# Kernel optimization log

Measured on AMD Instinct MI355X. Metric: run time of the kernel, lower is better.

Reference implementation:

```python
import jax, jax.numpy as jnp
import numpy as np

BATCH, SEQ, FEAT, LAYERS = 32, 512, 1024, 2


def setup_inputs() -> dict:
    key = jax.random.key(0)
    ks = jax.random.split(key, 1 + 3 * LAYERS)
    inp = {"x": jax.random.normal(ks[0], (BATCH, SEQ, FEAT), dtype=jnp.float32)}
    scale_i = 1.0 / np.sqrt(FEAT)
    for l in range(LAYERS):
        # flax OptimizedLSTMCell: input dense (no bias) + hidden dense (with bias),
        # both producing 4*features (gates i, f, g, o concatenated).
        inp[f"Wi{l}"] = jax.random.normal(ks[1 + 3 * l], (FEAT, 4 * FEAT), dtype=jnp.float32) * scale_i
        inp[f"Wh{l}"] = jax.random.normal(ks[2 + 3 * l], (FEAT, 4 * FEAT), dtype=jnp.float32) * scale_i
        inp[f"b{l}"] = jnp.zeros((4 * FEAT,), dtype=jnp.float32)
    return inp


def _lstm_layer(x, Wi, Wh, b):
    # x: [B, T, F_in]; returns [B, T, F]
    B = x.shape[0]
    F = Wh.shape[0]
    # Precompute input projections for all steps (one big GEMM): [B, T, 4F]
    xz = jnp.einsum("btf,fg->btg", x, Wi) + b

    def step(carry, xz_t):
        c, h = carry
        z = xz_t + h @ Wh  # [B, 4F]
        i, f, g, o = jnp.split(z, 4, axis=-1)
        c_new = jax.nn.sigmoid(f) * c + jax.nn.sigmoid(i) * jnp.tanh(g)
        h_new = jax.nn.sigmoid(o) * jnp.tanh(c_new)
        return (c_new, h_new), h_new

    init = (jnp.zeros((B, F), x.dtype), jnp.zeros((B, F), x.dtype))
    _, ys = jax.lax.scan(step, init, jnp.swapaxes(xz, 0, 1))  # scan over time
    return jnp.swapaxes(ys, 0, 1)


def reference(x, Wi0, Wh0, b0, Wi1, Wh1, b1):
    y = _lstm_layer(x, Wi0, Wh0, b0)
    y = _lstm_layer(y, Wi1, Wh1, b1)
    return y
```

## Files before the change

### kernel.cpp

```cpp
#include <hip/hip_runtime.h>
#include <hip/hip_bf16.h>
#include <hip/hip_fp16.h>


typedef _Float16 f16x8 __attribute__((ext_vector_type(8)));
typedef __fp16 fp16x2 __attribute__((ext_vector_type(2)));
typedef float f32x4 __attribute__((ext_vector_type(4)));

#define NB 32
#define NTT 512
#define NF 1024
#define NG 4096
#define TFE (NTT * NF)
#define NWG 256
#define NTHR 512

#define W_F16X8 8192
#define W_BYTES (W_F16X8 * 16)
#define ZQSEG 33
#define Z_FLOATS (8 * 16 * ZQSEG)
#define LDS_BYTES (W_BYTES + Z_FLOATS * 4)
#define RINGB 65536
#define MBOX 4096

__device__ __forceinline__ float sigm(float v) { return 1.0f / (1.0f + __expf(-v)); }
__device__ __forceinline__ float tanh_s(float v) {
  float a = fabsf(v);
  float e = __expf(-2.0f * a);
  float t = (1.0f - e) / (1.0f + e);
  return v < 0.0f ? -t : t;
}

__device__ __forceinline__ unsigned pk(float a, float b) {
  union { fp16x2 h2; unsigned u; } c;
  c.h2 = __builtin_amdgcn_cvt_pkrtz(a, b);
  return c.u;
}

__device__ __forceinline__ f16x8 cvt8(f32x4 lo, f32x4 hi) {
  union { unsigned u[4]; f16x8 h8; } u;
  u.u[0] = pk(lo[0], lo[1]);
  u.u[1] = pk(lo[2], lo[3]);
  u.u[2] = pk(hi[0], hi[1]);
  u.u[3] = pk(hi[2], hi[3]);
  return u.h8;
}

__device__ __forceinline__ unsigned ldu(const unsigned* p) {
  unsigned v;
  asm volatile("global_load_dword %0, %1, off sc0 sc1\n\ts_waitcnt vmcnt(0)"
               : "=&v"(v) : "v"(p) : "memory");
  return v;
}

__device__ __forceinline__ void ld4(f16x8 o[4], const char* p) {
  asm volatile("global_load_dwordx4 %0, %4, off sc0 sc1\n\t"
               "global_load_dwordx4 %1, %4, off offset:64 sc0 sc1\n\t"
               "global_load_dwordx4 %2, %4, off offset:128 sc0 sc1\n\t"
               "global_load_dwordx4 %3, %4, off offset:192 sc0 sc1"
               : "=&v"(o[0]), "=&v"(o[1]), "=&v"(o[2]), "=&v"(o[3])
               : "v"(p) : "memory");
}

__global__ __launch_bounds__(NTHR, 1) void lstm_persist(
    const float* __restrict__ x,
    const float* __restrict__ Wi0, const float* __restrict__ Wh0, const float* __restrict__ bv0,
    const float* __restrict__ Wi1, const float* __restrict__ Wh1, const float* __restrict__ bv1,
    float* __restrict__ out, unsigned short* __restrict__ hring_u16,
    unsigned* __restrict__ bar) {
  extern __shared__ char lds[];
  f16x8* Wl = (f16x8*)lds;
  float* Zr = (float*)(lds + W_BYTES);

  const int wg = blockIdx.x;
  const int tid = threadIdx.x;
  const int role = wg >> 7;
  const int fg = wg & 127;
  const int fbase = fg * 8;
  const int w = tid >> 6;
  const int Kq = w >> 1;
  const int mt = w & 1;
  const int lane = tid & 63;
  const int lr = lane & 15;
  const int g = lane >> 4;
  unsigned gen = 0;

  auto arrive = [&]() {
    asm volatile("s_waitcnt vmcnt(0) lgkmcnt(0)" ::: "memory");
    __syncthreads();
    ++gen;
    if (tid == 0)
      asm volatile("global_store_dword %0, %1, off sc0 sc1"
                   :: "v"(&bar[wg * 16]), "v"(gen) : "memory");
    if (wg == 0) {
      if (tid < 64) {
        const unsigned* f0 = &bar[(tid * 4 + 0) * 16];
        const unsigned* f1 = &bar[(tid * 4 + 1) * 16];
        const unsigned* f2 = &bar[(tid * 4 + 2) * 16];
        const unsigned* f3 = &bar[(tid * 4 + 3) * 16];
        for (;;) {
          unsigned v0, v1, v2, v3;
          asm volatile("global_load_dword %0, %4, off sc0 sc1\n\t"
                       "global_load_dword %1, %5, off sc0 sc1\n\t"
                       "global_load_dword %2, %6, off sc0 sc1\n\t"
                       "global_load_dword %3, %7, off sc0 sc1\n\t"
                       "s_waitcnt vmcnt(0)"
                       : "=&v"(v0), "=&v"(v1), "=&v"(v2), "=&v"(v3)
                       : "v"(f0), "v"(f1), "v"(f2), "v"(f3)
                       : "memory");
          if (__all((v0 >= gen) & (v1 >= gen) & (v2 >= gen) & (v3 >= gen))) break;
        }
      }
      __syncthreads();
      if (tid < 256)
        asm volatile("global_store_dword %0, %1, off sc0 sc1"
                     :: "v"(&bar[MBOX + tid * 16]), "v"(gen) : "memory");
      __syncthreads();
    }
  };

  auto waitgen = [&]() {
    const unsigned* mb = &bar[MBOX + wg * 16];
    for (;;) {
      if (ldu(mb) >= gen) break;
      __builtin_amdgcn_s_sleep(1);
    }
  };

  const float* Wi = role ? Wi1 : Wi0;
  const float* Wh = role ? Wh1 : Wh0;
  const float* bv = role ? bv1 : bv0;
  unsigned* h0 = (unsigned*)hring_u16;
  unsigned* h1 = (unsigned*)(hring_u16 + 2 * NB * NF);
  unsigned* hmine = role ? h1 : h0;

  for (int idx = tid; idx < 16384; idx += NTHR) {
    const int k = idx >> 3, chunk = idx & 7;
    const int q = chunk >> 1, half = chunk & 1;
    const float* src = (k < NF) ? (Wi + (size_t)k * NG) : (Wh + (size_t)(k - NF) * NG);
    const f32x4 v = *(const f32x4*)(src + q * NF + fbase + half * 4);
    const int s = k >> 5, kg = (k >> 3) & 3, jj = k & 7;
#pragma unroll
    for (int j = 0; j < 4; ++j) {
      const int c = q * 8 + half * 4 + j;
      _Float16* dst = (_Float16*)&Wl[((s * 2 + (c >> 4)) * 64) + kg * 16 + (c & 15)];
      dst[jj] = (_Float16)v[j];
    }
  }
  if (tid < 128) {
    const int b = tid >> 2, fp = tid & 3;
    __hip_atomic_store(&hmine[b * 512 + (fbase >> 1) + fp], 0u,
                       __ATOMIC_RELAXED, __HIP_MEMORY_SCOPE_AGENT);
  }
  float bias[4][2];
  if (tid < 128) {
    const int fp = tid & 3;
#pragma unroll
    for (int q = 0; q < 4; ++q) {
      bias[q][0] = bv[q * NF + fbase + 2 * fp];
      bias[q][1] = bv[q * NF + fbase + 2 * fp + 1];
    }
  }
  float cst[2] = {0.f, 0.f};
  __syncthreads();
  arrive();
  waitgen();

  for (int rd = 0; rd <= NTT; ++rd) {
    const bool doit = role == 0 ? (rd < NTT) : (rd >= 1);
    const int t = role == 0 ? rd : rd - 1;

    if (doit) {
      f32x4 acc0 = {0.f, 0.f, 0.f, 0.f}, acc1 = {0.f, 0.f, 0.f, 0.f};
      const int brow = mt * 16 + lr;

      if (role == 0 && w < 4) {
        const float* xp = x + (size_t)brow * TFE + (size_t)t * NF + Kq * 512 + g * 8;
#pragma unroll
        for (int ks = 0; ks < 16; ++ks) {
          const int s = Kq * 16 + ks;
          const f32x4 al = *(const f32x4*)(xp + ks * 32);
          const f32x4 ah = *(const f32x4*)(xp + ks * 32 + 4);
          const f16x8 A = cvt8(al, ah);
          acc0 = __builtin_amdgcn_mfma_f32_16x16x32_f16(A, Wl[(s * 2 + 0) * 64 + lane], acc0, 0, 0, 0);
          acc1 = __builtin_amdgcn_mfma_f32_16x16x32_f16(A, Wl[(s * 2 + 1) * 64 + lane], acc1, 0, 0, 0);
        }
      } else {
        waitgen();
        const char* hp;
        if (role == 0)
          hp = (const char*)h0 + (size_t)(rd & 1) * RINGB + brow * 2048
               + ((Kq - 2) * 512 + g * 8) * 2;
        else if (Kq < 2)
          hp = (const char*)h0 + (size_t)(rd & 1) * RINGB + brow * 2048
               + (Kq * 512 + g * 8) * 2;
        else
          hp = (const char*)h1 + (size_t)((rd + 1) & 1) * RINGB + brow * 2048
               + ((Kq - 2) * 512 + g * 8) * 2;

        f16x8 T[16];
        ld4(T + 0, hp);       ld4(T + 4, hp + 256);
        ld4(T + 8, hp + 512); ld4(T + 12, hp + 768);
        asm volatile("s_waitcnt vmcnt(12)" ::: "memory");
        __builtin_amdgcn_sched_barrier(0);
#pragma unroll
        for (int kk = 0; kk < 4; ++kk) {
          const int s = Kq * 16 + kk;
          acc0 = __builtin_amdgcn_mfma_f32_16x16x32_f16(T[kk], Wl[(s * 2 + 0) * 64 + lane], acc0, 0, 0, 0);
          acc1 = __builtin_amdgcn_mfma_f32_16x16x32_f16(T[kk], Wl[(s * 2 + 1) * 64 + lane], acc1, 0, 0, 0);
        }
        asm volatile("s_waitcnt vmcnt(8)" ::: "memory");
        __builtin_amdgcn_sched_barrier(0);
#pragma unroll
        for (int kk = 0; kk < 4; ++kk) {
          const int s = Kq * 16 + 4 + kk;
          acc0 = __builtin_amdgcn_mfma_f32_16x16x32_f16(T[4 + kk], Wl[(s * 2 + 0) * 64 + lane], acc0, 0, 0, 0);
          acc1 = __builtin_amdgcn_mfma_f32_16x16x32_f16(T[4 + kk], Wl[(s * 2 + 1) * 64 + lane], acc1, 0, 0, 0);
        }
        asm volatile("s_waitcnt vmcnt(4)" ::: "memory");
        __builtin_amdgcn_sched_barrier(0);
#pragma unroll
        for (int kk = 0; kk < 4; ++kk) {
          const int s = Kq * 16 + 8 + kk;
          acc0 = __builtin_amdgcn_mfma_f32_16x16x32_f16(T[8 + kk], Wl[(s * 2 + 0) * 64 + lane], acc0, 0, 0, 0);
          acc1 = __builtin_amdgcn_mfma_f32_16x16x32_f16(T[8 + kk], Wl[(s * 2 + 1) * 64 + lane], acc1, 0, 0, 0);
        }
        asm volatile("s_waitcnt vmcnt(0)" ::: "memory");
        __builtin_amdgcn_sched_barrier(0);
#pragma unroll
        for (int kk = 0; kk < 4; ++kk) {
          const int s = Kq * 16 + 12 + kk;
          acc0 = __builtin_amdgcn_mfma_f32_16x16x32_f16(T[12 + kk], Wl[(s * 2 + 0) * 64 + lane], acc0, 0, 0, 0);
          acc1 = __builtin_amdgcn_mfma_f32_16x16x32_f16(T[12 + kk], Wl[(s * 2 + 1) * 64 + lane], acc1, 0, 0, 0);
        }
      }

      {
        float* zb = Zr + (size_t)w * 16 * ZQSEG;
#pragma unroll
        for (int reg = 0; reg < 4; ++reg) {
          zb[(g * 4 + reg) * ZQSEG + lr] = acc0[reg];
          zb[(g * 4 + reg) * ZQSEG + 16 + lr] = acc1[reg];
        }
      }
    }
    __syncthreads();

    if (doit && tid < 128) {
      const int b = tid >> 2, fp = tid & 3;
      const int bmt = b >> 4, row = b & 15;
      float hv[2];
#pragma unroll
      for (int e = 0; e < 2; ++e) {
        const int f = 2 * fp + e;
        float zq[4];
#pragma unroll
        for (int q = 0; q < 4; ++q) {
          const int c = q * 8 + f;
          float sum = bias[q][e];
#pragma unroll
          for (int kq = 0; kq < 4; ++kq)
            sum += Zr[((kq * 2 + bmt) * 16 + row) * ZQSEG + c];
          zq[q] = sum;
        }
        const float cn = sigm(zq[1]) * cst[e] + sigm(zq[0]) * tanh_s(zq[2]);
        hv[e] = sigm(zq[3]) * tanh_s(cn);
        cst[e] = cn;
      }
      const int wph = role == 0 ? ((rd + 1) & 1) : (rd & 1);
      __hip_atomic_store(&hmine[wph * NB * 512 + b * 512 + (fbase >> 1) + fp],
                         pk(hv[0], hv[1]), __ATOMIC_RELAXED, __HIP_MEMORY_SCOPE_AGENT);
      if (role == 1)
        *(float2*)(out + (size_t)b * TFE + (size_t)t * NF + fbase + 2 * fp) =
            make_float2(hv[0], hv[1]);
    }
    arrive();
  }
}

extern "C" void kernel_launch(void* const* d_in, const int* in_sizes, int n_in,
                              void* d_out, int out_size, void* d_ws, size_t ws_size,
                              hipStream_t stream) {
  (void)in_sizes; (void)n_in; (void)out_size; (void)ws_size;
  const float* x   = (const float*)d_in[0];
  const float* Wi0 = (const float*)d_in[1];
  const float* Wh0 = (const float*)d_in[2];
  const float* b0  = (const float*)d_in[3];
  const float* Wi1 = (const float*)d_in[4];
  const float* Wh1 = (const float*)d_in[5];
  const float* b1  = (const float*)d_in[6];
  float* out = (float*)d_out;

  unsigned short* hring = (unsigned short*)d_ws;
  unsigned* bar = (unsigned*)((char*)d_ws + 262144);

  (void)hipMemsetAsync(bar, 0, 32768, stream);

  (void)hipFuncSetAttribute((const void*)lstm_persist,
                            hipFuncAttributeMaxDynamicSharedMemorySize, LDS_BYTES);

  lstm_persist<<<dim3(NWG), dim3(NTHR), LDS_BYTES, stream>>>(
      x, Wi0, Wh0, b0, Wi1, Wh1, b1, out, hring, bar);
}
```

Before: 3.896 ms.

## Split global barrier per layer and deepen hidden-state ring for decoupled layers

Replaces the single grid-wide barrier with two per-role barriers, each mastered by its own workgroup and publishing a separate generation counter into the mailbox. The hidden-state ring grows from two to eight slots per layer, and layer 1 runs three rounds behind layer 0 with explicit minimum-generation waits. Layer 0 no longer stalls on layer-1 workgroups each step, which is meant to cut barrier latency and let the two layers pipeline. The cost is a larger workspace and more intricate cross-role dependency tracking, where a wrong index could cause races.

```diff
diff --git a/kernel.cpp b/kernel.cpp
--- a/kernel.cpp
+++ b/kernel.cpp
@@ -21,6 +21,7 @@
 #define Z_FLOATS (8 * 16 * ZQSEG)
 #define LDS_BYTES (W_BYTES + Z_FLOATS * 4)
 #define RINGB 65536
+#define DEPTH 8
 #define MBOX 4096
 
 __device__ __forceinline__ float sigm(float v) { return 1.0f / (1.0f + __expf(-v)); }
@@ -44,13 +45,6 @@
   u.u[2] = pk(hi[0], hi[1]);
   u.u[3] = pk(hi[2], hi[3]);
   return u.h8;
-}
-
-__device__ __forceinline__ unsigned ldu(const unsigned* p) {
-  unsigned v;
-  asm volatile("global_load_dword %0, %1, off sc0 sc1\n\ts_waitcnt vmcnt(0)"
-               : "=&v"(v) : "v"(p) : "memory");
-  return v;
 }
 
 __device__ __forceinline__ void ld4(f16x8 o[4], const char* p) {
@@ -83,6 +77,7 @@
   const int lane = tid & 63;
   const int lr = lane & 15;
   const int g = lane >> 4;
+  const bool master = (fg == 0);
   unsigned gen = 0;
 
   auto arrive = [&]() {
@@ -92,37 +87,36 @@
     if (tid == 0)
       asm volatile("global_store_dword %0, %1, off sc0 sc1"
                    :: "v"(&bar[wg * 16]), "v"(gen) : "memory");
-    if (wg == 0) {
+    if (master) {
       if (tid < 64) {
-        const unsigned* f0 = &bar[(tid * 4 + 0) * 16];
-        const unsigned* f1 = &bar[(tid * 4 + 1) * 16];
-        const unsigned* f2 = &bar[(tid * 4 + 2) * 16];
-        const unsigned* f3 = &bar[(tid * 4 + 3) * 16];
+        const unsigned* fa = &bar[(role * 128 + 2 * tid) * 16];
+        const unsigned* fb = &bar[(role * 128 + 2 * tid + 1) * 16];
         for (;;) {
-          unsigned v0, v1, v2, v3;
-          asm volatile("global_load_dword %0, %4, off sc0 sc1\n\t"
-                       "global_load_dword %1, %5, off sc0 sc1\n\t"
-                       "global_load_dword %2, %6, off sc0 sc1\n\t"
-                       "global_load_dword %3, %7, off sc0 sc1\n\t"
+          unsigned v0, v1;
+          asm volatile("global_load_dword %0, %2, off sc0 sc1\n\t"
+                       "global_load_dword %1, %3, off sc0 sc1\n\t"
                        "s_waitcnt vmcnt(0)"
-                       : "=&v"(v0), "=&v"(v1), "=&v"(v2), "=&v"(v3)
-                       : "v"(f0), "v"(f1), "v"(f2), "v"(f3)
-                       : "memory");
-          if (__all((v0 >= gen) & (v1 >= gen) & (v2 >= gen) & (v3 >= gen))) break;
+                       : "=&v"(v0), "=&v"(v1) : "v"(fa), "v"(fb) : "memory");
+          if (__all((v0 >= gen) & (v1 >= gen))) break;
         }
       }
       __syncthreads();
       if (tid < 256)
         asm volatile("global_store_dword %0, %1, off sc0 sc1"
-                     :: "v"(&bar[MBOX + tid * 16]), "v"(gen) : "memory");
-      __syncthreads();
+                     :: "v"(&bar[MBOX + tid * 16 + role]), "v"(gen) : "memory");
     }
   };
 
-  auto waitgen = [&]() {
+  auto waitAB = [&](unsigned minA, unsigned minB) {
     const unsigned* mb = &bar[MBOX + wg * 16];
     for (;;) {
-      if (ldu(mb) >= gen) break;
+      unsigned a, b;
+      asm volatile("global_load_dwordx2 v[20:21], %2, off sc0 sc1\n\t"
+                   "s_waitcnt vmcnt(0)\n\t"
+                   "v_mov_b32 %0, v20\n\t"
+                   "v_mov_b32 %1, v21"
+                   : "=v"(a), "=v"(b) : "v"(mb) : "memory", "v20", "v21");
+      if (a >= minA && b >= minB) break;
       __builtin_amdgcn_s_sleep(1);
     }
   };
@@ -130,9 +124,9 @@
   const float* Wi = role ? Wi1 : Wi0;
   const float* Wh = role ? Wh1 : Wh0;
   const float* bv = role ? bv1 : bv0;
-  unsigned* h0 = (unsigned*)hring_u16;
-  unsigned* h1 = (unsigned*)(hring_u16 + 2 * NB * NF);
-  unsigned* hmine = role ? h1 : h0;
+  char* h0b = (char*)hring_u16;
+  char* h1b = (char*)hring_u16 + DEPTH * RINGB;
+  unsigned* hmine = (unsigned*)(role ? h1b : h0b);
 
   for (int idx = tid; idx < 16384; idx += NTHR) {
     const int k = idx >> 3, chunk = idx & 7;
@@ -164,11 +158,12 @@
   float cst[2] = {0.f, 0.f};
   __syncthreads();
   arrive();
-  waitgen();
-
-  for (int rd = 0; rd <= NTT; ++rd) {
-    const bool doit = role == 0 ? (rd < NTT) : (rd >= 1);
-    const int t = role == 0 ? rd : rd - 1;
+  waitAB(1, 1);
+
+  const int nrounds = role ? (NTT + 3) : NTT;
+  for (int rd = 0; rd < nrounds; ++rd) {
+    const bool doit = role == 0 ? true : (rd >= 3);
+    const int t = role == 0 ? rd : rd - 3;
 
     if (doit) {
       f32x4 acc0 = {0.f, 0.f, 0.f, 0.f}, acc1 = {0.f, 0.f, 0.f, 0.f};
@@ -186,17 +181,23 @@
           acc1 = __builtin_amdgcn_mfma_f32_16x16x32_f16(A, Wl[(s * 2 + 1) * 64 + lane], acc1, 0, 0, 0);
         }
       } else {
-        waitgen();
+        unsigned minA = 0, minB = 0;
         const char* hp;
-        if (role == 0)
-          hp = (const char*)h0 + (size_t)(rd & 1) * RINGB + brow * 2048
+        if (role == 0) {
+          minA = rd + 1;
+          minB = (rd >= 4) ? (unsigned)(rd - 3) : 0u;
+          hp = h0b + (size_t)(rd & 7) * RINGB + brow * 2048
                + ((Kq - 2) * 512 + g * 8) * 2;
-        else if (Kq < 2)
-          hp = (const char*)h0 + (size_t)(rd & 1) * RINGB + brow * 2048
+        } else if (Kq < 2) {
+          minA = rd - 1;
+          hp = h0b + (size_t)((rd - 2) & 7) * RINGB + brow * 2048
                + (Kq * 512 + g * 8) * 2;
-        else
-          hp = (const char*)h1 + (size_t)((rd + 1) & 1) * RINGB + brow * 2048
+        } else {
+          minB = (rd == 3) ? 1u : (unsigned)(rd + 1);
+          hp = h1b + (size_t)((rd - 3) & 7) * RINGB + brow * 2048
                + ((Kq - 2) * 512 + g * 8) * 2;
+        }
+        waitAB(minA, minB);
 
         f16x8 T[16];
         ld4(T + 0, hp);       ld4(T + 4, hp + 256);
@@ -267,8 +268,8 @@
         hv[e] = sigm(zq[3]) * tanh_s(cn);
         cst[e] = cn;
       }
-      const int wph = role == 0 ? ((rd + 1) & 1) : (rd & 1);
-      __hip_atomic_store(&hmine[wph * NB * 512 + b * 512 + (fbase >> 1) + fp],
+      const int wslot = (t + 1) & 7;
+      __hip_atomic_store(&hmine[(size_t)wslot * (RINGB / 4) + b * 512 + (fbase >> 1) + fp],
                          pk(hv[0], hv[1]), __ATOMIC_RELAXED, __HIP_MEMORY_SCOPE_AGENT);
       if (role == 1)
         *(float2*)(out + (size_t)b * TFE + (size_t)t * NF + fbase + 2 * fp) =
@@ -292,7 +293,7 @@
   float* out = (float*)d_out;
 
   unsigned short* hring = (unsigned short*)d_ws;
-  unsigned* bar = (unsigned*)((char*)d_ws + 262144);
+  unsigned* bar = (unsigned*)((char*)d_ws + 2 * DEPTH * RINGB);
 
   (void)hipMemsetAsync(bar, 0, 32768, stream);
 
```

Measured after the change: 3.878 ms. No clear change (-0.5%).
